# Performance work log

Hardware: AMD Instinct MI355X
Metric: run time of the kernel (lower is better)

## Reference

```python
import jax, jax.numpy as jnp
import numpy as np

B, DIN, H, DOUT, NB = 1024, 512, 1024, 512, 10
ALPHA = 0.5
INNER = 5


def setup_inputs() -> dict:
    key = jax.random.key(0)
    ks = jax.random.split(key, 5)
    return {
        "x": jax.random.normal(ks[0], (B, DIN), jnp.float32),
        "embed_W": jax.random.normal(ks[1], (H, DIN), jnp.float32) / np.float32(np.sqrt(DIN)),
        "embed_b": jnp.zeros((H,), jnp.float32),
        "block_W": jax.random.normal(ks[2], (NB, H, H), jnp.float32) * np.float32(0.8 / np.sqrt(H)),
        "block_b": jnp.zeros((NB, H), jnp.float32),
        "head_W": jax.random.normal(ks[3], (DOUT, H), jnp.float32) / np.float32(np.sqrt(H)),
        "head_b": jnp.zeros((DOUT,), jnp.float32),
        "steps": 30,
    }


def reference(x, embed_W, embed_b, block_W, block_b, head_W, head_b, steps):
    nb = block_W.shape[0]
    x_emb = x @ embed_W.T + embed_b  # [B, H]
    bb = block_b[:, None, :]  # [NB, 1, H]

    def inner_core(inp):
        # inp: [NB, B, H]; run inner equilibrium loop from h=0
        def body(h, _):
            pre = jnp.einsum('nbh,ndh->nbd', h, block_W) + bb + inp
            h = (1.0 - ALPHA) * h + ALPHA * jnp.tanh(pre)
            return h, None
        h, _ = jax.lax.scan(body, jnp.zeros_like(inp), None, length=INNER)
        return h

    def outer_step(h, _):
        # block i's input is previous-step state of block i-1 (block 0 gets x_emb)
        block_in = jnp.concatenate([x_emb[None], h[:-1]], axis=0)  # [NB, B, H]
        inner_eq = inner_core(h + block_in)
        h_new = (1.0 - ALPHA) * h + ALPHA * inner_eq
        return h_new, None

    h0 = jnp.zeros((nb,) + x_emb.shape, x_emb.dtype)
    h_final, _ = jax.lax.scan(outer_step, h0, None, length=steps)
    return h_final[-1] @ head_W.T + head_b  # [B, DOUT]
```

## Files before the change

kernel.cpp:

```cpp
#include <hip/hip_runtime.h>
#include <cstdint>
#include <cstddef>

#define B_DIM  1024
#define DIN    512
#define H_DIM  1024
#define DOUT   512
#define NB     10
#define STEPS  30

typedef _Float16 half_t;
typedef __attribute__((ext_vector_type(8))) _Float16 frag_ab;
typedef __attribute__((ext_vector_type(8))) _Float16 h8vec;
typedef __attribute__((ext_vector_type(4))) float    frag_cd;

__device__ __forceinline__ void gload16(const void* g, void* l) {
    __builtin_amdgcn_global_load_lds(
        (const __attribute__((address_space(1))) void*)g,
        (__attribute__((address_space(3))) void*)l, 16, 0, 0);
}

__device__ __forceinline__ float fast_tanh(float x) {
    float e, r;
    asm("v_exp_f32 %0, %1" : "=v"(e) : "v"(x * 2.8853900817779268f));
    asm("v_rcp_f32 %0, %1" : "=v"(r) : "v"(e + 1.0f));
    return __builtin_fmaf(-2.0f, r, 1.0f);
}

__global__ void __launch_bounds__(256)
f2h_kernel(const float* __restrict__ src, half_t* __restrict__ dst, int n4)
{
    const int i = blockIdx.x * 256 + threadIdx.x;
    if (i < n4) {
        const float4 v = ((const float4*)src)[i];
        half_t o[4] = { (half_t)v.x, (half_t)v.y, (half_t)v.z, (half_t)v.w };
        ((uint2*)dst)[i] = *(const uint2*)o;
    }
}

template <int MODE>
__global__ void __launch_bounds__(512, 4)
gemm_bt(const half_t* __restrict__ A,
        const half_t* __restrict__ W,
        const float* __restrict__ bias,
        const half_t* __restrict__ binp,
        const half_t* aux16,
        float* __restrict__ out32,
        half_t* out16,
        int M, int N, int K)
{
    __shared__ __attribute__((aligned(16))) char lds_raw[65536];
    half_t* lA  = (half_t*)lds_raw;
    half_t* lB  = (half_t*)(lds_raw + 32768);
    float*  fsm = (float*)lds_raw;

    const int tid  = threadIdx.x;
    const int wave = tid >> 6;
    const int lane = tid & 63;
    const int q    = lane >> 4;
    const int r16  = lane & 15;
    const int wm   = wave >> 2;
    const int wn   = wave & 3;

    const int srow = lane >> 3;
    const int scol = ((lane & 7) ^ srow) * 8;

    auto do_tile = [&](int bx, int by, int n) {
        const half_t* An = A + (size_t)n * M * K;
        const half_t* Wn = W + (size_t)n * N * K;
        const float*  bn = bias + (size_t)n * N;
        const half_t* binpn = binp;
        const half_t* auxn  = aux16;
        half_t* outn = out16;
        if (MODE != 0) {
            const size_t so = (size_t)n * M * N;
            binpn = binp + so;
            outn  = out16 + so;
            if (MODE == 2) auxn = aux16 + so;
        }
        const int tileM = by * 128;
        const int tileN = bx * 128;

        const half_t* gA = An + (size_t)(tileM + wave * 16 + srow) * K + scol;
        const half_t* gW = Wn + (size_t)(tileN + wave * 16 + srow) * K + scol;

        auto stage = [&](int k0, int b) {
#pragma unroll
            for (int i = 0; i < 2; ++i) {
                gload16(gA + (size_t)i * 8 * K + k0,
                        (void*)&lA[b * 8192 + (wave * 16 + i * 8) * 64]);
                gload16(gW + (size_t)i * 8 * K + k0,
                        (void*)&lB[b * 8192 + (wave * 16 + i * 8) * 64]);
            }
        };

        frag_cd acc[4][2];
#pragma unroll
        for (int mt = 0; mt < 4; ++mt)
#pragma unroll
            for (int nt = 0; nt < 2; ++nt)
                acc[mt][nt] = (frag_cd){0.f, 0.f, 0.f, 0.f};

        __syncthreads();
        const int NT = K >> 6;
        stage(0, 0);

        int cur = 0;
        for (int t = 0; t < NT; ++t) {
            if (t + 1 < NT) {
                stage((t + 1) << 6, cur ^ 1);
                asm volatile("s_waitcnt vmcnt(4)" ::: "memory");
            } else {
                asm volatile("s_waitcnt vmcnt(0)" ::: "memory");
            }
            __builtin_amdgcn_s_barrier();
            asm volatile("" ::: "memory");

            frag_ab av[2][4], bv[2][2];
#pragma unroll
            for (int kk = 0; kk < 2; ++kk) {
                const int cb = ((kk * 4 + q) ^ (r16 & 7)) * 8;
#pragma unroll
                for (int mt = 0; mt < 4; ++mt)
                    av[kk][mt] = *(const frag_ab*)&lA[cur * 8192 + (wm * 64 + mt * 16 + r16) * 64 + cb];
#pragma unroll
                for (int nt = 0; nt < 2; ++nt)
                    bv[kk][nt] = *(const frag_ab*)&lB[cur * 8192 + (wn * 32 + nt * 16 + r16) * 64 + cb];
            }
#pragma unroll
            for (int kk = 0; kk < 2; ++kk)
#pragma unroll
                for (int mt = 0; mt < 4; ++mt)
#pragma unroll
                    for (int nt = 0; nt < 2; ++nt)
                        acc[mt][nt] = __builtin_amdgcn_mfma_f32_16x16x32_f16(
                            av[kk][mt], bv[kk][nt], acc[mt][nt], 0, 0, 0);

            asm volatile("" ::: "memory");
            __builtin_amdgcn_s_barrier();
            cur ^= 1;
        }

        if (MODE == 0) {
#pragma unroll
            for (int mt = 0; mt < 4; ++mt)
#pragma unroll
                for (int nt = 0; nt < 2; ++nt)
#pragma unroll
                    for (int r = 0; r < 4; ++r) {
                        const int row = tileM + wm * 64 + mt * 16 + q * 4 + r;
                        const int col = tileN + wn * 32 + nt * 16 + r16;
                        out32[(size_t)row * N + col] = acc[mt][nt][r] + bn[col];
                    }
            return;
        }

#pragma unroll
        for (int mt = 0; mt < 4; ++mt)
#pragma unroll
            for (int nt = 0; nt < 2; ++nt)
#pragma unroll
                for (int r = 0; r < 4; ++r) {
                    const int row = wm * 64 + mt * 16 + q * 4 + r;
                    const int col = wn * 32 + nt * 16 + r16;
                    const int g   = col >> 2;
                    const int gl  = (g & 24) | ((g ^ (g >> 3) ^ (row & 7)) & 7);
                    fsm[row * 128 + gl * 4 + (col & 3)] = acc[mt][nt][r];
                }
        __syncthreads();

#pragma unroll
        for (int c = 0; c < 4; ++c) {
            const int e   = (c * 512 + tid) * 8;
            const int rl  = e >> 7;
            const int cl  = e & 127;
            const int row = tileM + rl;
            const int col = tileN + cl;
            const size_t gidx = (size_t)row * N + col;

            const int g0  = cl >> 2;
            const int gl0 = (g0 & 24) | ((g0 ^ (g0 >> 3) ^ (rl & 7)) & 7);
            const int g1  = g0 + 1;
            const int gl1 = (g1 & 24) | ((g1 ^ (g1 >> 3) ^ (rl & 7)) & 7);
            const float4 va = *(const float4*)&fsm[rl * 128 + gl0 * 4];
            const float4 vb = *(const float4*)&fsm[rl * 128 + gl1 * 4];
            const float vv[8] = {va.x, va.y, va.z, va.w, vb.x, vb.y, vb.z, vb.w};

            const h8vec bi8 = *(const h8vec*)&binpn[gidx];
            h8vec ho8, ax8;
            ho8 = *(const h8vec*)&An[(size_t)row * K + col];
            if (MODE == 2) ax8 = *(const h8vec*)&auxn[gidx];

            half_t o[8];
#pragma unroll
            for (int j = 0; j < 8; ++j) {
                const float bi = (float)bi8[j];
                const float tt = fast_tanh(vv[j] + bi);
                const float ho = (float)ho8[j];
                const float hn = 0.5f * ho + 0.5f * tt;
                const float ov = (MODE == 2) ? 0.5f * (float)ax8[j] + 0.5f * hn : hn;
                o[j] = (half_t)ov;
            }
            *(uint4*)&outn[gidx] = *(const uint4*)o;
        }
    };

    if (MODE == 0) {
        const int gx  = gridDim.x, gy = gridDim.y;
        const int nwg = gx * gy * gridDim.z;
        const int f   = blockIdx.x + gx * (blockIdx.y + gy * blockIdx.z);
        const int w   = (f & 7) * (nwg >> 3) + (f >> 3);
        const int bx  = w % gx;
        const int rst = w / gx;
        do_tile(bx, rst % gy, rst / gy);
    } else {
        const int f   = blockIdx.x;
        const int xcd = f & 7;
        const int j   = f >> 3;
        const int w1  = xcd * 80 + j;
        do_tile(w1 & 7, (w1 >> 3) & 7, w1 >> 6);
        if (j < 16) {
            const int w2 = xcd * 80 + 64 + j;
            do_tile(w2 & 7, (w2 >> 3) & 7, w2 >> 6);
        }
    }
}

__global__ void __launch_bounds__(256)
pre_outer_kernel(const half_t* __restrict__ h,
                 const float* __restrict__ x_emb,
                 const float* __restrict__ bb,
                 half_t* __restrict__ binp,
                 half_t* __restrict__ hhh)
{
    const int f  = blockIdx.x;
    const int k  = f & 7;
    const int j  = f >> 3;
    const int p  = 10 * k + (j % 10);
    const int bi = j / 10;
    const int n  = p >> 3;

    const size_t idx = ((size_t)p << 17) + (size_t)bi * 2048 + (size_t)threadIdx.x * 8;
    const size_t off = idx - (size_t)n * B_DIM * H_DIM;
    const int    col = (int)(off & (H_DIM - 1));

    const h8vec ha = *(const h8vec*)&h[idx];
    float pv[8];
    if (n == 0) {
        const float4 p0 = *(const float4*)&x_emb[off];
        const float4 p1 = *(const float4*)&x_emb[off + 4];
        pv[0] = p0.x; pv[1] = p0.y; pv[2] = p0.z; pv[3] = p0.w;
        pv[4] = p1.x; pv[5] = p1.y; pv[6] = p1.z; pv[7] = p1.w;
    } else {
        const h8vec pa = *(const h8vec*)&h[idx - (size_t)B_DIM * H_DIM];
#pragma unroll
        for (int j2 = 0; j2 < 8; ++j2) pv[j2] = (float)pa[j2];
    }
    const float4 b0 = *(const float4*)&bb[(size_t)n * H_DIM + col];
    const float4 b1 = *(const float4*)&bb[(size_t)n * H_DIM + col + 4];
    const float bp[8] = {b0.x, b0.y, b0.z, b0.w, b1.x, b1.y, b1.z, b1.w};

    half_t bv[8], hv[8];
#pragma unroll
    for (int j2 = 0; j2 < 8; ++j2) {
        const float biv = (float)ha[j2] + pv[j2] + bp[j2];
        bv[j2] = (half_t)biv;
        hv[j2] = (half_t)(0.5f * fast_tanh(biv));
    }
    *(uint4*)&binp[idx] = *(const uint4*)bv;
    *(uint4*)&hhh[idx]  = *(const uint4*)hv;
}

static inline void conv(const float* src, half_t* dst, int n, hipStream_t s) {
    const int n4 = n / 4;
    f2h_kernel<<<(n4 + 255) / 256, 256, 0, s>>>(src, dst, n4);
}

extern "C" void kernel_launch(void* const* d_in, const int* in_sizes, int n_in,
                              void* d_out, int out_size, void* d_ws, size_t ws_size,
                              hipStream_t stream)
{
    const float* x     = (const float*)d_in[0];
    const float* embW  = (const float*)d_in[1];
    const float* embB  = (const float*)d_in[2];
    const float* blkW  = (const float*)d_in[3];
    const float* blkB  = (const float*)d_in[4];
    const float* headW = (const float*)d_in[5];
    const float* headB = (const float*)d_in[6];
    float* out = (float*)d_out;

    char* ws = (char*)d_ws;
    size_t off = 0;
    auto alloc = [&](size_t bytes) {
        void* p = ws + off;
        off += (bytes + 255) & ~(size_t)255;
        return p;
    };
    const size_t NE = (size_t)NB * B_DIM * H_DIM;

    float* xemb32 = (float*)alloc((size_t)B_DIM * H_DIM * 4);
    half_t* h16    = (half_t*)alloc(NE * 2);
    half_t* binp16 = (half_t*)alloc(NE * 2);
    half_t* hhh0   = (half_t*)alloc(NE * 2);
    half_t* hhh1   = (half_t*)alloc(NE * 2);
    half_t* wx     = (half_t*)alloc((size_t)B_DIM * DIN * 2);
    half_t* wembW  = (half_t*)alloc((size_t)H_DIM * DIN * 2);
    half_t* wblkW  = (half_t*)alloc((size_t)NB * H_DIM * H_DIM * 2);
    half_t* wheadW = (half_t*)alloc((size_t)DOUT * H_DIM * 2);
    (void)ws_size;

    conv(x,     wx,     B_DIM * DIN,        stream);
    conv(embW,  wembW,  H_DIM * DIN,        stream);
    conv(blkW,  wblkW,  NB * H_DIM * H_DIM, stream);
    conv(headW, wheadW, DOUT * H_DIM,       stream);

    hipMemsetAsync(h16, 0, NE * 2, stream);

    const dim3 blk(512);

    gemm_bt<0><<<dim3(H_DIM / 128, B_DIM / 128, 1), blk, 0, stream>>>(
        wx, wembW, embB, nullptr, nullptr, xemb32, nullptr, B_DIM, H_DIM, DIN);

    const int ggrid = 512;
    const int pre_blocks = (int)(NE / (8 * 256));
    for (int s = 0; s < STEPS; ++s) {
        pre_outer_kernel<<<pre_blocks, dim3(256), 0, stream>>>(h16, xemb32, blkB,
                                                               binp16, hhh0);
        gemm_bt<1><<<ggrid, blk, 0, stream>>>(hhh0, wblkW, blkB, binp16, nullptr,
                                              nullptr, hhh1, B_DIM, H_DIM, H_DIM);
        gemm_bt<1><<<ggrid, blk, 0, stream>>>(hhh1, wblkW, blkB, binp16, nullptr,
                                              nullptr, hhh0, B_DIM, H_DIM, H_DIM);
        gemm_bt<1><<<ggrid, blk, 0, stream>>>(hhh0, wblkW, blkB, binp16, nullptr,
                                              nullptr, hhh1, B_DIM, H_DIM, H_DIM);
        gemm_bt<2><<<ggrid, blk, 0, stream>>>(hhh1, wblkW, blkB, binp16, h16,
                                              nullptr, h16, B_DIM, H_DIM, H_DIM);
    }

    gemm_bt<0><<<dim3(DOUT / 128, B_DIM / 128, 1), blk, 0, stream>>>(
        h16 + (size_t)(NB - 1) * B_DIM * H_DIM, wheadW, headB, nullptr, nullptr,
        out, nullptr, B_DIM, DOUT, H_DIM);
}
```

Baseline: 4.240 ms.

## Enlarge GEMM tiles to 256x256 with 1024-thread blocks and one tile per block

```diff
diff --git a/kernel.cpp b/kernel.cpp
--- a/kernel.cpp
+++ b/kernel.cpp
@@ -39,7 +39,7 @@
 }
 
 template <int MODE>
-__global__ void __launch_bounds__(512, 4)
+__global__ void __launch_bounds__(1024, 4)
 gemm_bt(const half_t* __restrict__ A,
         const half_t* __restrict__ W,
         const float* __restrict__ bias,
@@ -49,10 +49,10 @@
         half_t* out16,
         int M, int N, int K)
 {
-    __shared__ __attribute__((aligned(16))) char lds_raw[65536];
-    half_t* lA  = (half_t*)lds_raw;
-    half_t* lB  = (half_t*)(lds_raw + 32768);
-    float*  fsm = (float*)lds_raw;
+    extern __shared__ char smem[];
+    half_t* lA  = (half_t*)smem;
+    half_t* lB  = (half_t*)(smem + 65536);
+    float*  fsm = (float*)smem;
 
     const int tid  = threadIdx.x;
     const int wave = tid >> 6;
@@ -78,8 +78,8 @@
             outn  = out16 + so;
             if (MODE == 2) auxn = aux16 + so;
         }
-        const int tileM = by * 128;
-        const int tileN = bx * 128;
+        const int tileM = by * 256;
+        const int tileN = bx * 256;
 
         const half_t* gA = An + (size_t)(tileM + wave * 16 + srow) * K + scol;
         const half_t* gW = Wn + (size_t)(tileN + wave * 16 + srow) * K + scol;
@@ -88,20 +88,19 @@
 #pragma unroll
             for (int i = 0; i < 2; ++i) {
                 gload16(gA + (size_t)i * 8 * K + k0,
-                        (void*)&lA[b * 8192 + (wave * 16 + i * 8) * 64]);
+                        (void*)&lA[b * 16384 + (wave * 16 + i * 8) * 64]);
                 gload16(gW + (size_t)i * 8 * K + k0,
-                        (void*)&lB[b * 8192 + (wave * 16 + i * 8) * 64]);
+                        (void*)&lB[b * 16384 + (wave * 16 + i * 8) * 64]);
             }
         };
 
-        frag_cd acc[4][2];
+        frag_cd acc[4][4];
 #pragma unroll
         for (int mt = 0; mt < 4; ++mt)
 #pragma unroll
-            for (int nt = 0; nt < 2; ++nt)
+            for (int nt = 0; nt < 4; ++nt)
                 acc[mt][nt] = (frag_cd){0.f, 0.f, 0.f, 0.f};
 
-        __syncthreads();
         const int NT = K >> 6;
         stage(0, 0);
 
@@ -116,23 +115,23 @@
             __builtin_amdgcn_s_barrier();
             asm volatile("" ::: "memory");
 
-            frag_ab av[2][4], bv[2][2];
+            frag_ab av[2][4], bv[2][4];
 #pragma unroll
             for (int kk = 0; kk < 2; ++kk) {
                 const int cb = ((kk * 4 + q) ^ (r16 & 7)) * 8;
 #pragma unroll
                 for (int mt = 0; mt < 4; ++mt)
-                    av[kk][mt] = *(const frag_ab*)&lA[cur * 8192 + (wm * 64 + mt * 16 + r16) * 64 + cb];
-#pragma unroll
-                for (int nt = 0; nt < 2; ++nt)
-                    bv[kk][nt] = *(const frag_ab*)&lB[cur * 8192 + (wn * 32 + nt * 16 + r16) * 64 + cb];
+                    av[kk][mt] = *(const frag_ab*)&lA[cur * 16384 + (wm * 64 + mt * 16 + r16) * 64 + cb];
+#pragma unroll
+                for (int nt = 0; nt < 4; ++nt)
+                    bv[kk][nt] = *(const frag_ab*)&lB[cur * 16384 + (wn * 64 + nt * 16 + r16) * 64 + cb];
             }
 #pragma unroll
             for (int kk = 0; kk < 2; ++kk)
 #pragma unroll
                 for (int mt = 0; mt < 4; ++mt)
 #pragma unroll
-                    for (int nt = 0; nt < 2; ++nt)
+                    for (int nt = 0; nt < 4; ++nt)
                         acc[mt][nt] = __builtin_amdgcn_mfma_f32_16x16x32_f16(
                             av[kk][mt], bv[kk][nt], acc[mt][nt], 0, 0, 0);
 
@@ -145,63 +144,68 @@
 #pragma unroll
             for (int mt = 0; mt < 4; ++mt)
 #pragma unroll
-                for (int nt = 0; nt < 2; ++nt)
+                for (int nt = 0; nt < 4; ++nt)
 #pragma unroll
                     for (int r = 0; r < 4; ++r) {
                         const int row = tileM + wm * 64 + mt * 16 + q * 4 + r;
-                        const int col = tileN + wn * 32 + nt * 16 + r16;
+                        const int col = tileN + wn * 64 + nt * 16 + r16;
                         out32[(size_t)row * N + col] = acc[mt][nt][r] + bn[col];
                     }
             return;
         }
 
-#pragma unroll
-        for (int mt = 0; mt < 4; ++mt)
-#pragma unroll
-            for (int nt = 0; nt < 2; ++nt)
-#pragma unroll
-                for (int r = 0; r < 4; ++r) {
-                    const int row = wm * 64 + mt * 16 + q * 4 + r;
-                    const int col = wn * 32 + nt * 16 + r16;
-                    const int g   = col >> 2;
-                    const int gl  = (g & 24) | ((g ^ (g >> 3) ^ (row & 7)) & 7);
-                    fsm[row * 128 + gl * 4 + (col & 3)] = acc[mt][nt][r];
+        for (int pass = 0; pass < 2; ++pass) {
+            __syncthreads();
+            if ((wm >> 1) == pass) {
+#pragma unroll
+                for (int mt = 0; mt < 4; ++mt)
+#pragma unroll
+                    for (int nt = 0; nt < 4; ++nt)
+#pragma unroll
+                        for (int r = 0; r < 4; ++r) {
+                            const int rl  = (wm & 1) * 64 + mt * 16 + q * 4 + r;
+                            const int col = wn * 64 + nt * 16 + r16;
+                            const int g   = col >> 2;
+                            const int gl  = (g & 56) | ((g ^ (g >> 3) ^ (rl & 7)) & 7);
+                            fsm[rl * 256 + gl * 4 + (col & 3)] = acc[mt][nt][r];
+                        }
+            }
+            __syncthreads();
+
+#pragma unroll
+            for (int c = 0; c < 4; ++c) {
+                const int e   = (c * 1024 + tid) * 8;
+                const int rl  = e >> 8;
+                const int cl  = e & 255;
+                const int row = tileM + pass * 128 + rl;
+                const int col = tileN + cl;
+                const size_t gidx = (size_t)row * N + col;
+
+                const int g0  = cl >> 2;
+                const int gl0 = (g0 & 56) | ((g0 ^ (g0 >> 3) ^ (rl & 7)) & 7);
+                const int g1  = g0 + 1;
+                const int gl1 = (g1 & 56) | ((g1 ^ (g1 >> 3) ^ (rl & 7)) & 7);
+                const float4 va = *(const float4*)&fsm[rl * 256 + gl0 * 4];
+                const float4 vb = *(const float4*)&fsm[rl * 256 + gl1 * 4];
+                const float vv[8] = {va.x, va.y, va.z, va.w, vb.x, vb.y, vb.z, vb.w};
+
+                const h8vec bi8 = *(const h8vec*)&binpn[gidx];
+                h8vec ho8, ax8;
+                ho8 = *(const h8vec*)&An[(size_t)row * K + col];
+                if (MODE == 2) ax8 = *(const h8vec*)&auxn[gidx];
+
+                half_t o[8];
+#pragma unroll
+                for (int j = 0; j < 8; ++j) {
+                    const float bi = (float)bi8[j];
+                    const float tt = fast_tanh(vv[j] + bi);
+                    const float ho = (float)ho8[j];
+                    const float hn = 0.5f * ho + 0.5f * tt;
+                    const float ov = (MODE == 2) ? 0.5f * (float)ax8[j] + 0.5f * hn : hn;
+                    o[j] = (half_t)ov;
                 }
-        __syncthreads();
-
-#pragma unroll
-        for (int c = 0; c < 4; ++c) {
-            const int e   = (c * 512 + tid) * 8;
-            const int rl  = e >> 7;
-            const int cl  = e & 127;
-            const int row = tileM + rl;
-            const int col = tileN + cl;
-            const size_t gidx = (size_t)row * N + col;
-
-            const int g0  = cl >> 2;
-            const int gl0 = (g0 & 24) | ((g0 ^ (g0 >> 3) ^ (rl & 7)) & 7);
-            const int g1  = g0 + 1;
-            const int gl1 = (g1 & 24) | ((g1 ^ (g1 >> 3) ^ (rl & 7)) & 7);
-            const float4 va = *(const float4*)&fsm[rl * 128 + gl0 * 4];
-            const float4 vb = *(const float4*)&fsm[rl * 128 + gl1 * 4];
-            const float vv[8] = {va.x, va.y, va.z, va.w, vb.x, vb.y, vb.z, vb.w};
-
-            const h8vec bi8 = *(const h8vec*)&binpn[gidx];
-            h8vec ho8, ax8;
-            ho8 = *(const h8vec*)&An[(size_t)row * K + col];
-            if (MODE == 2) ax8 = *(const h8vec*)&auxn[gidx];
-
-            half_t o[8];
-#pragma unroll
-            for (int j = 0; j < 8; ++j) {
-                const float bi = (float)bi8[j];
-                const float tt = fast_tanh(vv[j] + bi);
-                const float ho = (float)ho8[j];
-                const float hn = 0.5f * ho + 0.5f * tt;
-                const float ov = (MODE == 2) ? 0.5f * (float)ax8[j] + 0.5f * hn : hn;
-                o[j] = (half_t)ov;
-            }
-            *(uint4*)&outn[gidx] = *(const uint4*)o;
+                *(uint4*)&outn[gidx] = *(const uint4*)o;
+            }
         }
     };
 
@@ -215,14 +219,8 @@
         do_tile(bx, rst % gy, rst / gy);
     } else {
         const int f   = blockIdx.x;
-        const int xcd = f & 7;
-        const int j   = f >> 3;
-        const int w1  = xcd * 80 + j;
-        do_tile(w1 & 7, (w1 >> 3) & 7, w1 >> 6);
-        if (j < 16) {
-            const int w2 = xcd * 80 + 64 + j;
-            do_tile(w2 & 7, (w2 >> 3) & 7, w2 >> 6);
-        }
+        const int w   = (f & 7) * 20 + (f >> 3);
+        do_tile(w & 3, (w >> 2) & 3, w >> 4);
     }
 }
 
@@ -236,11 +234,11 @@
     const int f  = blockIdx.x;
     const int k  = f & 7;
     const int j  = f >> 3;
-    const int p  = 10 * k + (j % 10);
-    const int bi = j / 10;
-    const int n  = p >> 3;
-
-    const size_t idx = ((size_t)p << 17) + (size_t)bi * 2048 + (size_t)threadIdx.x * 8;
+    const int p  = 5 * k + (j % 5);
+    const int bi = j / 5;
+    const int n  = p >> 2;
+
+    const size_t idx = ((size_t)p << 18) + (size_t)bi * 2048 + (size_t)threadIdx.x * 8;
     const size_t off = idx - (size_t)n * B_DIM * H_DIM;
     const int    col = (int)(off & (H_DIM - 1));
 
@@ -316,27 +314,28 @@
 
     hipMemsetAsync(h16, 0, NE * 2, stream);
 
-    const dim3 blk(512);
-
-    gemm_bt<0><<<dim3(H_DIM / 128, B_DIM / 128, 1), blk, 0, stream>>>(
+    const dim3 blk(1024);
+    const size_t shmem = 131072;
+
+    gemm_bt<0><<<dim3(H_DIM / 256, B_DIM / 256, 1), blk, shmem, stream>>>(
         wx, wembW, embB, nullptr, nullptr, xemb32, nullptr, B_DIM, H_DIM, DIN);
 
-    const int ggrid = 512;
+    const int ggrid = 160;
     const int pre_blocks = (int)(NE / (8 * 256));
     for (int s = 0; s < STEPS; ++s) {
         pre_outer_kernel<<<pre_blocks, dim3(256), 0, stream>>>(h16, xemb32, blkB,
                                                                binp16, hhh0);
-        gemm_bt<1><<<ggrid, blk, 0, stream>>>(hhh0, wblkW, blkB, binp16, nullptr,
-                                              nullptr, hhh1, B_DIM, H_DIM, H_DIM);
-        gemm_bt<1><<<ggrid, blk, 0, stream>>>(hhh1, wblkW, blkB, binp16, nullptr,
-                                              nullptr, hhh0, B_DIM, H_DIM, H_DIM);
-        gemm_bt<1><<<ggrid, blk, 0, stream>>>(hhh0, wblkW, blkB, binp16, nullptr,
-                                              nullptr, hhh1, B_DIM, H_DIM, H_DIM);
-        gemm_bt<2><<<ggrid, blk, 0, stream>>>(hhh1, wblkW, blkB, binp16, h16,
-                                              nullptr, h16, B_DIM, H_DIM, H_DIM);
-    }
-
-    gemm_bt<0><<<dim3(DOUT / 128, B_DIM / 128, 1), blk, 0, stream>>>(
+        gemm_bt<1><<<ggrid, blk, shmem, stream>>>(hhh0, wblkW, blkB, binp16, nullptr,
+                                                  nullptr, hhh1, B_DIM, H_DIM, H_DIM);
+        gemm_bt<1><<<ggrid, blk, shmem, stream>>>(hhh1, wblkW, blkB, binp16, nullptr,
+                                                  nullptr, hhh0, B_DIM, H_DIM, H_DIM);
+        gemm_bt<1><<<ggrid, blk, shmem, stream>>>(hhh0, wblkW, blkB, binp16, nullptr,
+                                                  nullptr, hhh1, B_DIM, H_DIM, H_DIM);
+        gemm_bt<2><<<ggrid, blk, shmem, stream>>>(hhh1, wblkW, blkB, binp16, h16,
+                                                  nullptr, h16, B_DIM, H_DIM, H_DIM);
+    }
+
+    gemm_bt<0><<<dim3(DOUT / 256, B_DIM / 256, 1), blk, shmem, stream>>>(
         h16 + (size_t)(NB - 1) * B_DIM * H_DIM, wheadW, headB, nullptr, nullptr,
         out, nullptr, B_DIM, DOUT, H_DIM);
 }
```

New measurement: 6.922 ms. +63.2%, slower.

## Split K across wave halves with 64x64 wave tiles and LDS reduction

Applied to the files above, without the earlier changes.

```diff
diff --git a/kernel.cpp b/kernel.cpp
--- a/kernel.cpp
+++ b/kernel.cpp
@@ -59,8 +59,9 @@
     const int lane = tid & 63;
     const int q    = lane >> 4;
     const int r16  = lane & 15;
-    const int wm   = wave >> 2;
-    const int wn   = wave & 3;
+    const int kh   = wave >> 2;
+    const int wm   = (wave >> 1) & 1;
+    const int wn   = wave & 1;
 
     const int srow = lane >> 3;
     const int scol = ((lane & 7) ^ srow) * 8;
@@ -94,11 +95,11 @@
             }
         };
 
-        frag_cd acc[4][2];
+        frag_cd acc[4][4];
 #pragma unroll
         for (int mt = 0; mt < 4; ++mt)
 #pragma unroll
-            for (int nt = 0; nt < 2; ++nt)
+            for (int nt = 0; nt < 4; ++nt)
                 acc[mt][nt] = (frag_cd){0.f, 0.f, 0.f, 0.f};
 
         __syncthreads();
@@ -116,57 +117,55 @@
             __builtin_amdgcn_s_barrier();
             asm volatile("" ::: "memory");
 
-            frag_ab av[2][4], bv[2][2];
-#pragma unroll
-            for (int kk = 0; kk < 2; ++kk) {
-                const int cb = ((kk * 4 + q) ^ (r16 & 7)) * 8;
-#pragma unroll
-                for (int mt = 0; mt < 4; ++mt)
-                    av[kk][mt] = *(const frag_ab*)&lA[cur * 8192 + (wm * 64 + mt * 16 + r16) * 64 + cb];
-#pragma unroll
-                for (int nt = 0; nt < 2; ++nt)
-                    bv[kk][nt] = *(const frag_ab*)&lB[cur * 8192 + (wn * 32 + nt * 16 + r16) * 64 + cb];
-            }
-#pragma unroll
-            for (int kk = 0; kk < 2; ++kk)
-#pragma unroll
-                for (int mt = 0; mt < 4; ++mt)
-#pragma unroll
-                    for (int nt = 0; nt < 2; ++nt)
-                        acc[mt][nt] = __builtin_amdgcn_mfma_f32_16x16x32_f16(
-                            av[kk][mt], bv[kk][nt], acc[mt][nt], 0, 0, 0);
+            const int cb = ((kh * 4 + q) ^ (r16 & 7)) * 8;
+            frag_ab av[4], bv[4];
+#pragma unroll
+            for (int mt = 0; mt < 4; ++mt)
+                av[mt] = *(const frag_ab*)&lA[cur * 8192 + (wm * 64 + mt * 16 + r16) * 64 + cb];
+#pragma unroll
+            for (int nt = 0; nt < 4; ++nt)
+                bv[nt] = *(const frag_ab*)&lB[cur * 8192 + (wn * 64 + nt * 16 + r16) * 64 + cb];
+#pragma unroll
+            for (int mt = 0; mt < 4; ++mt)
+#pragma unroll
+                for (int nt = 0; nt < 4; ++nt)
+                    acc[mt][nt] = __builtin_amdgcn_mfma_f32_16x16x32_f16(
+                        av[mt], bv[nt], acc[mt][nt], 0, 0, 0);
 
             asm volatile("" ::: "memory");
             __builtin_amdgcn_s_barrier();
             cur ^= 1;
         }
 
-        if (MODE == 0) {
+        if (kh == 1) {
 #pragma unroll
             for (int mt = 0; mt < 4; ++mt)
 #pragma unroll
-                for (int nt = 0; nt < 2; ++nt)
+                for (int nt = 0; nt < 4; ++nt)
 #pragma unroll
                     for (int r = 0; r < 4; ++r) {
-                        const int row = tileM + wm * 64 + mt * 16 + q * 4 + r;
-                        const int col = tileN + wn * 32 + nt * 16 + r16;
-                        out32[(size_t)row * N + col] = acc[mt][nt][r] + bn[col];
+                        const int row = wm * 64 + mt * 16 + q * 4 + r;
+                        const int col = wn * 64 + nt * 16 + r16;
+                        const int g   = col >> 2;
+                        const int gl  = (g & 24) | ((g ^ (g >> 3) ^ (row & 7)) & 7);
+                        fsm[row * 128 + gl * 4 + (col & 3)] = acc[mt][nt][r];
                     }
-            return;
-        }
-
-#pragma unroll
-        for (int mt = 0; mt < 4; ++mt)
-#pragma unroll
-            for (int nt = 0; nt < 2; ++nt)
-#pragma unroll
-                for (int r = 0; r < 4; ++r) {
-                    const int row = wm * 64 + mt * 16 + q * 4 + r;
-                    const int col = wn * 32 + nt * 16 + r16;
-                    const int g   = col >> 2;
-                    const int gl  = (g & 24) | ((g ^ (g >> 3) ^ (row & 7)) & 7);
-                    fsm[row * 128 + gl * 4 + (col & 3)] = acc[mt][nt][r];
-                }
+        }
+        __syncthreads();
+        if (kh == 0) {
+#pragma unroll
+            for (int mt = 0; mt < 4; ++mt)
+#pragma unroll
+                for (int nt = 0; nt < 4; ++nt)
+#pragma unroll
+                    for (int r = 0; r < 4; ++r) {
+                        const int row = wm * 64 + mt * 16 + q * 4 + r;
+                        const int col = wn * 64 + nt * 16 + r16;
+                        const int g   = col >> 2;
+                        const int gl  = (g & 24) | ((g ^ (g >> 3) ^ (row & 7)) & 7);
+                        fsm[row * 128 + gl * 4 + (col & 3)] += acc[mt][nt][r];
+                    }
+        }
         __syncthreads();
 
 #pragma unroll
@@ -186,22 +185,31 @@
             const float4 vb = *(const float4*)&fsm[rl * 128 + gl1 * 4];
             const float vv[8] = {va.x, va.y, va.z, va.w, vb.x, vb.y, vb.z, vb.w};
 
-            const h8vec bi8 = *(const h8vec*)&binpn[gidx];
-            h8vec ho8, ax8;
-            ho8 = *(const h8vec*)&An[(size_t)row * K + col];
-            if (MODE == 2) ax8 = *(const h8vec*)&auxn[gidx];
-
-            half_t o[8];
-#pragma unroll
-            for (int j = 0; j < 8; ++j) {
-                const float bi = (float)bi8[j];
-                const float tt = fast_tanh(vv[j] + bi);
-                const float ho = (float)ho8[j];
-                const float hn = 0.5f * ho + 0.5f * tt;
-                const float ov = (MODE == 2) ? 0.5f * (float)ax8[j] + 0.5f * hn : hn;
-                o[j] = (half_t)ov;
+            if (MODE == 0) {
+                const float4 b0 = *(const float4*)&bn[col];
+                const float4 b1 = *(const float4*)&bn[col + 4];
+                float4 o0 = {vv[0] + b0.x, vv[1] + b0.y, vv[2] + b0.z, vv[3] + b0.w};
+                float4 o1 = {vv[4] + b1.x, vv[5] + b1.y, vv[6] + b1.z, vv[7] + b1.w};
+                *(float4*)&out32[gidx]     = o0;
+                *(float4*)&out32[gidx + 4] = o1;
+            } else {
+                const h8vec bi8 = *(const h8vec*)&binpn[gidx];
+                h8vec ho8, ax8;
+                ho8 = *(const h8vec*)&An[(size_t)row * K + col];
+                if (MODE == 2) ax8 = *(const h8vec*)&auxn[gidx];
+
+                half_t o[8];
+#pragma unroll
+                for (int j = 0; j < 8; ++j) {
+                    const float bi = (float)bi8[j];
+                    const float tt = fast_tanh(vv[j] + bi);
+                    const float ho = (float)ho8[j];
+                    const float hn = 0.5f * ho + 0.5f * tt;
+                    const float ov = (MODE == 2) ? 0.5f * (float)ax8[j] + 0.5f * hn : hn;
+                    o[j] = (half_t)ov;
+                }
+                *(uint4*)&outn[gidx] = *(const uint4*)o;
             }
-            *(uint4*)&outn[gidx] = *(const uint4*)o;
         }
     };
 
```

New measurement: 4.876 ms. 15.0% more time.
